# Performance work log

Hardware: AMD Instinct MI355X
Metric: run time of the kernel (lower is better)

## Reference

```python
import jax, jax.numpy as jnp
import numpy as np

N_HEAD = 16
LN_EPS = 1e-5


def setup_inputs() -> dict:
    key = jax.random.key(0)
    ks = jax.random.split(key, 12)
    B, S, D = 4, 1024, 1024
    s = 1.0 / np.sqrt(D)
    return {
        "Q": jax.random.normal(ks[0], (B, S, D), jnp.float32),
        "K": jax.random.normal(ks[1], (B, S, D), jnp.float32),
        "V": jax.random.normal(ks[2], (B, S, D), jnp.float32),
        # Linear weights stored torch-style [out, in]
        "Wq": jax.random.normal(ks[3], (D, D), jnp.float32) * s,
        "bq": jnp.zeros((D,), jnp.float32),
        "Wk": jax.random.normal(ks[4], (D, D), jnp.float32) * s,
        "bk": jnp.zeros((D,), jnp.float32),
        "Wv": jax.random.normal(ks[5], (D, D), jnp.float32) * s,
        "bv": jnp.zeros((D,), jnp.float32),
        "Wo": jax.random.normal(ks[6], (D, D), jnp.float32) * s,
        "bo": jnp.zeros((D,), jnp.float32),
        "ln_g": jnp.ones((D,), jnp.float32),
        "ln_b": jnp.zeros((D,), jnp.float32),
    }


def _layer_norm(x, g, b):
    mu = jnp.mean(x, axis=-1, keepdims=True)
    var = jnp.mean(jnp.square(x - mu), axis=-1, keepdims=True)
    return (x - mu) * jax.lax.rsqrt(var + LN_EPS) * g + b


def reference(Q, K, V, Wq, bq, Wk, bk, Wv, bv, Wo, bo, ln_g, ln_b):
    B, S, D = Q.shape
    H = N_HEAD
    dk = D // H
    # projections, split heads: [B, H, S, dk]
    q = (Q @ Wq.T + bq).reshape(B, S, H, dk).transpose(0, 2, 1, 3)
    k = (K @ Wk.T + bk).reshape(B, S, H, dk).transpose(0, 2, 1, 3)
    v = (V @ Wv.T + bv).reshape(B, S, H, dk).transpose(0, 2, 1, 3)
    scores = jnp.einsum("bhqd,bhkd->bhqk", q, k) / np.sqrt(dk)
    # NOTE: original module applies softmax twice (F.softmax then nn.Softmax)
    attn = jax.nn.softmax(jax.nn.softmax(scores, axis=-1), axis=-1)
    ctx = jnp.einsum("bhqk,bhkd->bhqd", attn, v)  # [B, H, S, dk]
    ctx = ctx.transpose(0, 2, 1, 3).reshape(B, S, D)
    out = ctx @ Wo.T + bo
    return _layer_norm(out + Q, ln_g, ln_b)
```

## Files before the change

### kernel.cpp

```cpp
#include <hip/hip_runtime.h>
#include <cstdint>
#include <cstddef>


typedef unsigned short ushort_t;
typedef __attribute__((ext_vector_type(8))) short bf16x8;
typedef __attribute__((ext_vector_type(8))) unsigned short us8;
typedef __attribute__((ext_vector_type(4))) unsigned short us4;
typedef __attribute__((ext_vector_type(4))) float f32x4;

#define MFMA16(a, b, c) __builtin_amdgcn_mfma_f32_16x16x32_bf16((a), (b), (c), 0, 0, 0)
#define EXP2F(x) __builtin_amdgcn_exp2f(x)
#define LOG2E 1.4426950408889634f

__device__ __forceinline__ float b2f(ushort_t u) {
  union { unsigned int i; float f; } x; x.i = ((unsigned int)u) << 16; return x.f;
}
__device__ __forceinline__ ushort_t f2b(float f) {
  union { unsigned int i; float f; } x; x.f = f;
  unsigned int r = (x.i + 0x7FFFu + ((x.i >> 16) & 1u)) >> 16;
  return (ushort_t)r;
}
__device__ __forceinline__ unsigned int cvtpk(float lo, float hi) {
  unsigned int r;
  asm("v_cvt_pk_bf16_f32 %0, %1, %2" : "=v"(r) : "v"(lo), "v"(hi));
  return r;
}
__device__ __forceinline__ us8 cvt8pk(float4 a, float4 b) {
  union { unsigned int u[4]; us8 v; } r;
  r.u[0] = cvtpk(a.x, a.y); r.u[1] = cvtpk(a.z, a.w);
  r.u[2] = cvtpk(b.x, b.y); r.u[3] = cvtpk(b.z, b.w);
  return r.v;
}

__device__ __forceinline__ void gll16(const ushort_t* g, ushort_t* l) {
  __builtin_amdgcn_global_load_lds(
      (const __attribute__((address_space(1))) void*)g,
      (__attribute__((address_space(3))) void*)l, 16, 0, 0);
}

__global__ __launch_bounds__(256, 8) void cvt4_kernel(
    const float* __restrict__ w0, const float* __restrict__ w1,
    const float* __restrict__ w2, const float* __restrict__ w3,
    ushort_t* __restrict__ dst) {
  const int which = blockIdx.y;
  const float* src = (which == 0) ? w0 : (which == 1) ? w1 : (which == 2) ? w2 : w3;
  const int i = (blockIdx.x * 256 + threadIdx.x) * 8;
  const float4 a = *(const float4*)(src + i);
  const float4 b = *(const float4*)(src + i + 4);
  *(us8*)(dst + (size_t)which * 1048576 + i) = cvt8pk(a, b);
}

__global__ __launch_bounds__(256, 3) void qkv_proj_kernel(
    const float* __restrict__ Qin, const float* __restrict__ Kin,
    const float* __restrict__ Vin,
    const ushort_t* __restrict__ wq, const ushort_t* __restrict__ wk,
    const ushort_t* __restrict__ wv,
    const float* __restrict__ bq, const float* __restrict__ bk,
    const float* __restrict__ bv,
    ushort_t* __restrict__ qb, ushort_t* __restrict__ kb,
    ushort_t* __restrict__ vb) {
  __shared__ __align__(16) ushort_t Asl0[128 * 32];
  __shared__ __align__(16) ushort_t Asl1[128 * 32];
  __shared__ __align__(16) ushort_t Bsl[3][128 * 32];
  const float* A; const ushort_t* W; const float* bias; float scale;
  if (blockIdx.z == 0)      { A = Qin; W = wq; bias = bq; scale = 0.125f * LOG2E; }
  else if (blockIdx.z == 1) { A = Kin; W = wk; bias = bk; scale = 1.0f; }
  else                      { A = Vin; W = wv; bias = bv; scale = 1.0f; }
  const int l = blockIdx.x;
  const int xcd = l & 7, ii = l >> 3;
  const int m0 = (xcd * 4 + (ii >> 3)) * 128;
  const int n0 = (ii & 7) * 128;
  const int tid = threadIdx.x;
  const int wave = tid >> 6, lane = tid & 63;
  const int l15 = lane & 15, quad = lane >> 4;
  const int wr = wave >> 1, wc = wave & 1;

  const int ra = tid >> 2, ca = (tid & 3) * 8;
  const float* Ap0 = A + (size_t)(m0 + ra) * 1024 + ca;
  const float* Ap1 = A + (size_t)(m0 + ra + 64) * 1024 + ca;

  const ushort_t* Bg0 = W + (size_t)(n0 + wave * 32 + (lane >> 2)) * 1024 + (lane & 3) * 8;
  const ushort_t* Bg1 = W + (size_t)(n0 + wave * 32 + 16 + (lane >> 2)) * 1024 + (lane & 3) * 8;
  ushort_t* Ba = Bsl[0];
  ushort_t* Bb = Bsl[1];
  ushort_t* Bc = Bsl[2];

  float4 xa0 = *(const float4*)(Ap0), xa1 = *(const float4*)(Ap0 + 4);
  float4 xa2 = *(const float4*)(Ap1), xa3 = *(const float4*)(Ap1 + 4);
  gll16(Bg0, Ba + wave * 1024);
  gll16(Bg1, Ba + wave * 1024 + 512);
  gll16(Bg0 + 32, Bb + wave * 1024);
  gll16(Bg1 + 32, Bb + wave * 1024 + 512);
  float4 ya0 = *(const float4*)(Ap0 + 32), ya1 = *(const float4*)(Ap0 + 36);
  float4 ya2 = *(const float4*)(Ap1 + 32), ya3 = *(const float4*)(Ap1 + 36);
  *(us8*)(Asl0 + ra * 32 + ca) = cvt8pk(xa0, xa1);
  *(us8*)(Asl0 + (ra + 64) * 32 + ca) = cvt8pk(xa2, xa3);
  asm volatile("s_waitcnt vmcnt(6) lgkmcnt(0)" ::: "memory");
  __builtin_amdgcn_s_barrier();

  f32x4 acc[4][4] = {};
#define QKV_COMPUTE(ASL, BSL)                                                   \
  {                                                                             \
    bf16x8 af[4], bfr[4];                                                       \
    _Pragma("unroll") for (int s = 0; s < 4; ++s)                               \
        af[s] = *(const bf16x8*)((ASL) + (wr * 64 + s * 16 + l15) * 32 + quad * 8); \
    _Pragma("unroll") for (int s = 0; s < 4; ++s)                               \
        bfr[s] = *(const bf16x8*)((BSL) + (wc * 64 + s * 16 + l15) * 32 + quad * 8); \
    _Pragma("unroll") for (int ms = 0; ms < 4; ++ms)                            \
        _Pragma("unroll") for (int ns = 0; ns < 4; ++ns)                        \
            acc[ms][ns] = MFMA16(af[ms], bfr[ns], acc[ms][ns]);                 \
  }

  for (int i = 0; i < 15; ++i) {
    const int k0 = i * 64;
    gll16(Bg0 + k0 + 64, Bc + wave * 1024);
    gll16(Bg1 + k0 + 64, Bc + wave * 1024 + 512);
    xa0 = *(const float4*)(Ap0 + k0 + 64); xa1 = *(const float4*)(Ap0 + k0 + 68);
    xa2 = *(const float4*)(Ap1 + k0 + 64); xa3 = *(const float4*)(Ap1 + k0 + 68);
    QKV_COMPUTE(Asl0, Ba)
    *(us8*)(Asl1 + ra * 32 + ca) = cvt8pk(ya0, ya1);
    *(us8*)(Asl1 + (ra + 64) * 32 + ca) = cvt8pk(ya2, ya3);
    asm volatile("s_waitcnt vmcnt(6) lgkmcnt(0)" ::: "memory");
    __builtin_amdgcn_s_barrier();
    gll16(Bg0 + k0 + 96, Ba + wave * 1024);
    gll16(Bg1 + k0 + 96, Ba + wave * 1024 + 512);
    ya0 = *(const float4*)(Ap0 + k0 + 96); ya1 = *(const float4*)(Ap0 + k0 + 100);
    ya2 = *(const float4*)(Ap1 + k0 + 96); ya3 = *(const float4*)(Ap1 + k0 + 100);
    QKV_COMPUTE(Asl1, Bb)
    *(us8*)(Asl0 + ra * 32 + ca) = cvt8pk(xa0, xa1);
    *(us8*)(Asl0 + (ra + 64) * 32 + ca) = cvt8pk(xa2, xa3);
    asm volatile("s_waitcnt vmcnt(6) lgkmcnt(0)" ::: "memory");
    __builtin_amdgcn_s_barrier();
    ushort_t* t = Ba; Ba = Bc; Bc = Bb; Bb = t;
  }
  QKV_COMPUTE(Asl0, Ba)
  *(us8*)(Asl1 + ra * 32 + ca) = cvt8pk(ya0, ya1);
  *(us8*)(Asl1 + (ra + 64) * 32 + ca) = cvt8pk(ya2, ya3);
  asm volatile("s_waitcnt vmcnt(0) lgkmcnt(0)" ::: "memory");
  __builtin_amdgcn_s_barrier();
  QKV_COMPUTE(Asl1, Bb)
#undef QKV_COMPUTE

  if (blockIdx.z != 2) {
    ushort_t* outp = (blockIdx.z == 0) ? qb : kb;
#pragma unroll
    for (int ns = 0; ns < 4; ++ns) {
      const int col = n0 + wc * 64 + ns * 16 + l15;
      const float bv_ = bias[col];
#pragma unroll
      for (int ms = 0; ms < 4; ++ms) {
        const int rowb = m0 + wr * 64 + ms * 16 + quad * 4;
#pragma unroll
        for (int r = 0; r < 4; ++r) {
          outp[(size_t)(rowb + r) * 1024 + col] =
              f2b((acc[ms][ns][r] + bv_) * scale);
        }
      }
    }
  } else {
#pragma unroll
    for (int ns = 0; ns < 4; ++ns) {
      const int col = n0 + wc * 64 + ns * 16 + l15;
      const float bv_ = bias[col];
      const int h = col >> 6, d = col & 63;
#pragma unroll
      for (int ms = 0; ms < 4; ++ms) {
        const int i0 = m0 + wr * 64 + ms * 16 + quad * 4;
        const int b = i0 >> 10, s0 = i0 & 1023;
        us4 pack;
#pragma unroll
        for (int r = 0; r < 4; ++r) pack[r] = f2b(acc[ms][ns][r] + bv_);
        *(us4*)(vb + ((size_t)(b * 16 + h) * 64 + d) * 1024 + s0) = pack;
      }
    }
  }
}

__global__ __launch_bounds__(256, 4) void attn_kernel(
    const ushort_t* __restrict__ qb, const ushort_t* __restrict__ kb,
    const ushort_t* __restrict__ vb, ushort_t* __restrict__ ctx) {
  __shared__ __align__(16) ushort_t Sh0[64 * 72];
  __shared__ __align__(16) ushort_t Sh1[64 * 72];
  __shared__ __align__(16) ushort_t Sh2[64 * 72];
  __shared__ __align__(16) ushort_t Sh3[64 * 72];

  const int tid = threadIdx.x, wave = tid >> 6, lane = tid & 63;
  const int l15 = lane & 15, quad = lane >> 4;
  const int l = blockIdx.x;
  const int xcd = l & 7, ii = l >> 3;
  const int bh = xcd * 8 + (ii >> 4);
  const int q0 = (ii & 15) * 64;
  const int b = bh >> 4, h = bh & 15;
  const ushort_t* qg = qb + ((size_t)b << 20) + h * 64;
  const ushort_t* kg = kb + ((size_t)b << 20) + h * 64;
  const ushort_t* vg = vb + ((size_t)bh << 16);

  const int kr0 = tid >> 3, kc0 = (tid & 7) * 8;
  const int kr1 = (tid + 256) >> 3, kc1 = kc0;
  const int o0 = kr0 * 72 + kc0, o1 = kr1 * 72 + kc1;

  *(us8*)(Sh0 + o0) = *(const us8*)(qg + (size_t)(q0 + kr0) * 1024 + kc0);
  *(us8*)(Sh0 + o1) = *(const us8*)(qg + (size_t)(q0 + kr1) * 1024 + kc1);
  us8 rk0 = *(const us8*)(kg + (size_t)kr0 * 1024 + kc0);
  us8 rk1 = *(const us8*)(kg + (size_t)kr1 * 1024 + kc1);
  *(us8*)(Sh1 + o0) = rk0;
  *(us8*)(Sh1 + o1) = rk1;
  rk0 = *(const us8*)(kg + (size_t)(64 + kr0) * 1024 + kc0);
  rk1 = *(const us8*)(kg + (size_t)(64 + kr1) * 1024 + kc1);
  __syncthreads();
  bf16x8 aqh[2];
  aqh[0] = *(const bf16x8*)(Sh0 + (wave * 16 + l15) * 72 + quad * 8);
  aqh[1] = *(const bf16x8*)(Sh0 + (wave * 16 + l15) * 72 + 32 + quad * 8);

  float z1 = 0.f;
  for (int kt = 0; kt < 16; ++kt) {
    const ushort_t* kcur = (kt & 1) ? Sh2 : Sh1;
    f32x4 sc[4] = {};
#pragma unroll
    for (int kk = 0; kk < 2; ++kk) {
#pragma unroll
      for (int ns = 0; ns < 4; ++ns) {
        const bf16x8 kf = *(const bf16x8*)(kcur + (ns * 16 + l15) * 72 + kk * 32 + quad * 8);
        sc[ns] = MFMA16(kf, aqh[kk], sc[ns]);
      }
    }
    if (kt < 15) {
      ushort_t* knxt = (kt & 1) ? Sh1 : Sh2;
      *(us8*)(knxt + o0) = rk0;
      *(us8*)(knxt + o1) = rk1;
      if (kt < 14) {
        rk0 = *(const us8*)(kg + (size_t)((kt + 2) * 64 + kr0) * 1024 + kc0);
        rk1 = *(const us8*)(kg + (size_t)((kt + 2) * 64 + kr1) * 1024 + kc1);
      }
    }
#pragma unroll
    for (int ns = 0; ns < 4; ++ns)
#pragma unroll
      for (int r = 0; r < 4; ++r) z1 += EXP2F(sc[ns][r]);
    asm volatile("s_waitcnt lgkmcnt(0)" ::: "memory");
    __builtin_amdgcn_s_barrier();
  }
  z1 += __shfl_xor(z1, 16, 64);
  z1 += __shfl_xor(z1, 32, 64);
  const float iz1 = LOG2E / z1;

  const int adr0 = ((((quad & 1) << 1) * 16) + l15) << 2;
  const int adr1 = adr0 + 64;

  f32x4 oac[4] = {};
  float z2 = 0.f;
  rk0 = *(const us8*)(kg + (size_t)kr0 * 1024 + kc0);
  rk1 = *(const us8*)(kg + (size_t)kr1 * 1024 + kc1);
  us8 rv0 = *(const us8*)(vg + (size_t)kr0 * 1024 + kc0);
  us8 rv1 = *(const us8*)(vg + (size_t)kr1 * 1024 + kc1);
  *(us8*)(Sh0 + o0) = rk0;
  *(us8*)(Sh0 + o1) = rk1;
  *(us8*)(Sh2 + o0) = rv0;
  *(us8*)(Sh2 + o1) = rv1;
  rk0 = *(const us8*)(kg + (size_t)(64 + kr0) * 1024 + kc0);
  rk1 = *(const us8*)(kg + (size_t)(64 + kr1) * 1024 + kc1);
  rv0 = *(const us8*)(vg + (size_t)kr0 * 1024 + 64 + kc0);
  rv1 = *(const us8*)(vg + (size_t)kr1 * 1024 + 64 + kc1);
  asm volatile("s_waitcnt lgkmcnt(0)" ::: "memory");
  __builtin_amdgcn_s_barrier();

  for (int kt = 0; kt < 16; ++kt) {
    const ushort_t* kcur = (kt & 1) ? Sh1 : Sh0;
    const ushort_t* vcur = (kt & 1) ? Sh3 : Sh2;
    f32x4 sc[4] = {};
#pragma unroll
    for (int kk = 0; kk < 2; ++kk) {
#pragma unroll
      for (int ns = 0; ns < 4; ++ns) {
        const bf16x8 kf = *(const bf16x8*)(kcur + (ns * 16 + l15) * 72 + kk * 32 + quad * 8);
        sc[ns] = MFMA16(kf, aqh[kk], sc[ns]);
      }
    }
    if (kt < 15) {
      ushort_t* knxt = (kt & 1) ? Sh0 : Sh1;
      ushort_t* vnxt = (kt & 1) ? Sh2 : Sh3;
      *(us8*)(knxt + o0) = rk0;
      *(us8*)(knxt + o1) = rk1;
      *(us8*)(vnxt + o0) = rv0;
      *(us8*)(vnxt + o1) = rv1;
      if (kt < 14) {
        rk0 = *(const us8*)(kg + (size_t)((kt + 2) * 64 + kr0) * 1024 + kc0);
        rk1 = *(const us8*)(kg + (size_t)((kt + 2) * 64 + kr1) * 1024 + kc1);
        rv0 = *(const us8*)(vg + (size_t)kr0 * 1024 + (kt + 2) * 64 + kc0);
        rv1 = *(const us8*)(vg + (size_t)kr1 * 1024 + (kt + 2) * 64 + kc1);
      }
    }
    unsigned int D[4][2];
#pragma unroll
    for (int ns = 0; ns < 4; ++ns) {
      const float e0 = EXP2F(EXP2F(sc[ns][0]) * iz1);
      const float e1 = EXP2F(EXP2F(sc[ns][1]) * iz1);
      const float e2 = EXP2F(EXP2F(sc[ns][2]) * iz1);
      const float e3 = EXP2F(EXP2F(sc[ns][3]) * iz1);
      z2 += (e0 + e1) + (e2 + e3);
      D[ns][0] = cvtpk(e0, e1);
      D[ns][1] = cvtpk(e2, e3);
    }
#pragma unroll
    for (int kk = 0; kk < 2; ++kk) {
      union { unsigned int u[4]; bf16x8 v; } pf;
#pragma unroll
      for (int t = 0; t < 4; ++t) {
        const int adr = (t >> 1) ? adr1 : adr0;
        const int lo = __builtin_amdgcn_ds_bpermute(adr, (int)D[2 * kk][t & 1]);
        const int hi = __builtin_amdgcn_ds_bpermute(adr, (int)D[2 * kk + 1][t & 1]);
        pf.u[t] = (unsigned int)((quad >= 2) ? hi : lo);
      }
#pragma unroll
      for (int ns2 = 0; ns2 < 4; ++ns2) {
        const bf16x8 vf = *(const bf16x8*)(vcur + (ns2 * 16 + l15) * 72 + kk * 32 + quad * 8);
        oac[ns2] = MFMA16(vf, pf.v, oac[ns2]);
      }
    }
    asm volatile("s_waitcnt lgkmcnt(0)" ::: "memory");
    __builtin_amdgcn_s_barrier();
  }

  z2 += __shfl_xor(z2, 16, 64);
  z2 += __shfl_xor(z2, 32, 64);
  const int s = q0 + wave * 16 + l15;
  ushort_t* crow = ctx + ((size_t)(b * 1024 + s)) * 1024 + h * 64;
#pragma unroll
  for (int ns2 = 0; ns2 < 4; ++ns2) {
    us4 pack;
#pragma unroll
    for (int r = 0; r < 4; ++r) pack[r] = f2b(oac[ns2][r] / z2);
    *(us4*)(crow + ns2 * 16 + quad * 4) = pack;
  }
}

__global__ __launch_bounds__(256, 4) void out_proj_kernel(
    const ushort_t* __restrict__ ctxp, const ushort_t* __restrict__ wo,
    const float* __restrict__ bo, ushort_t* __restrict__ pre) {
  __shared__ __align__(16) ushort_t Abuf[3][64 * 32];
  __shared__ __align__(16) ushort_t Bbuf[3][128 * 32];
  const int tid = threadIdx.x;
  const int wave = tid >> 6, lane = tid & 63;
  const int l15 = lane & 15, quad = lane >> 4;
  const int wr = wave >> 1, wc = wave & 1;
  const int l = blockIdx.x;
  const int xcd = l & 7, ii = l >> 3;
  const int m0 = (xcd * 8 + (ii >> 3)) * 64;
  const int n0 = (ii & 7) * 128;

  const ushort_t* Ag = ctxp + (size_t)(m0 + wave * 16 + (lane >> 2)) * 1024 + (lane & 3) * 8;
  const ushort_t* Bg0 = wo + (size_t)(n0 + wave * 32 + (lane >> 2)) * 1024 + (lane & 3) * 8;
  const ushort_t* Bg1 = wo + (size_t)(n0 + wave * 32 + 16 + (lane >> 2)) * 1024 + (lane & 3) * 8;

  ushort_t* Aa = Abuf[0]; ushort_t* Ab = Abuf[1]; ushort_t* Ac = Abuf[2];
  ushort_t* Ba = Bbuf[0]; ushort_t* Bb = Bbuf[1]; ushort_t* Bc = Bbuf[2];

  gll16(Ag, Aa + wave * 512);
  gll16(Bg0, Ba + wave * 1024);
  gll16(Bg1, Ba + wave * 1024 + 512);
  gll16(Ag + 32, Ab + wave * 512);
  gll16(Bg0 + 32, Bb + wave * 1024);
  gll16(Bg1 + 32, Bb + wave * 1024 + 512);
  asm volatile("s_waitcnt vmcnt(3)" ::: "memory");
  __builtin_amdgcn_s_barrier();

  f32x4 acc[2][4] = {};
#define OUTP_COMPUTE(ASL, BSL)                                                  \
  {                                                                             \
    bf16x8 af[2], bfr[4];                                                       \
    _Pragma("unroll") for (int s = 0; s < 2; ++s)                               \
        af[s] = *(const bf16x8*)((ASL) + (wr * 32 + s * 16 + l15) * 32 + quad * 8); \
    _Pragma("unroll") for (int s = 0; s < 4; ++s)                               \
        bfr[s] = *(const bf16x8*)((BSL) + (wc * 64 + s * 16 + l15) * 32 + quad * 8); \
    _Pragma("unroll") for (int ms = 0; ms < 2; ++ms)                            \
        _Pragma("unroll") for (int ns = 0; ns < 4; ++ns)                        \
            acc[ms][ns] = MFMA16(af[ms], bfr[ns], acc[ms][ns]);                 \
  }

  for (int p = 0; p < 30; ++p) {
    const int k = p * 32;
    gll16(Ag + k + 64, Ac + wave * 512);
    gll16(Bg0 + k + 64, Bc + wave * 1024);
    gll16(Bg1 + k + 64, Bc + wave * 1024 + 512);
    OUTP_COMPUTE(Aa, Ba)
    asm volatile("s_waitcnt vmcnt(3) lgkmcnt(0)" ::: "memory");
    __builtin_amdgcn_s_barrier();
    ushort_t* ta = Aa; Aa = Ab; Ab = Ac; Ac = ta;
    ushort_t* tb = Ba; Ba = Bb; Bb = Bc; Bc = tb;
  }
  OUTP_COMPUTE(Aa, Ba)
  asm volatile("s_waitcnt vmcnt(0) lgkmcnt(0)" ::: "memory");
  __builtin_amdgcn_s_barrier();
  OUTP_COMPUTE(Ab, Bb)
#undef OUTP_COMPUTE

#pragma unroll
  for (int ns = 0; ns < 4; ++ns) {
    const int col = n0 + wc * 64 + ns * 16 + l15;
    const float bv_ = bo[col];
#pragma unroll
    for (int ms = 0; ms < 2; ++ms) {
      const int rowb = m0 + wr * 32 + ms * 16 + quad * 4;
#pragma unroll
      for (int r = 0; r < 4; ++r) {
        pre[(size_t)(rowb + r) * 1024 + col] = f2b(acc[ms][ns][r] + bv_);
      }
    }
  }
}

__global__ __launch_bounds__(256, 4) void ln_kernel(
    const ushort_t* __restrict__ pre, const float* __restrict__ Q,
    const float* __restrict__ g, const float* __restrict__ bta,
    float* __restrict__ out) {
  const int row = blockIdx.x;
  const int tid = threadIdx.x;
  const size_t base = (size_t)row * 1024 + tid * 4;
  const ushort4 p4 = *(const ushort4*)(pre + base);
  const float4 q4 = *(const float4*)(Q + base);
  float v[4] = {b2f(p4.x) + q4.x, b2f(p4.y) + q4.y,
                b2f(p4.z) + q4.z, b2f(p4.w) + q4.w};
  float s1 = v[0] + v[1] + v[2] + v[3];
  float s2 = v[0]*v[0] + v[1]*v[1] + v[2]*v[2] + v[3]*v[3];
#pragma unroll
  for (int off = 1; off < 64; off <<= 1) {
    s1 += __shfl_xor(s1, off, 64);
    s2 += __shfl_xor(s2, off, 64);
  }
  __shared__ float r1[4], r2[4];
  const int wave = tid >> 6, lane = tid & 63;
  if (lane == 0) { r1[wave] = s1; r2[wave] = s2; }
  __syncthreads();
  const float t1 = r1[0] + r1[1] + r1[2] + r1[3];
  const float t2 = r2[0] + r2[1] + r2[2] + r2[3];
  const float mu = t1 * (1.0f / 1024.0f);
  const float var = t2 * (1.0f / 1024.0f) - mu * mu;
  const float inv = rsqrtf(var + 1e-5f);
  const int c0 = tid * 4;
#pragma unroll
  for (int j = 0; j < 4; ++j) {
    const int c = c0 + j;
    out[(size_t)row * 1024 + c] = (v[j] - mu) * inv * g[c] + bta[c];
  }
}

extern "C" void kernel_launch(void* const* d_in, const int* in_sizes, int n_in,
                              void* d_out, int out_size, void* d_ws, size_t ws_size,
                              hipStream_t stream) {
  const float* Q  = (const float*)d_in[0];
  const float* K  = (const float*)d_in[1];
  const float* V  = (const float*)d_in[2];
  const float* Wq = (const float*)d_in[3];
  const float* bq = (const float*)d_in[4];
  const float* Wk = (const float*)d_in[5];
  const float* bk = (const float*)d_in[6];
  const float* Wv = (const float*)d_in[7];
  const float* bv = (const float*)d_in[8];
  const float* Wo = (const float*)d_in[9];
  const float* bo = (const float*)d_in[10];
  const float* lg = (const float*)d_in[11];
  const float* lb = (const float*)d_in[12];

  char* ws = (char*)d_ws;
  ushort_t* qb  = (ushort_t*)(ws);
  ushort_t* kb  = (ushort_t*)(ws + ((size_t)8  << 20));
  ushort_t* vb  = (ushort_t*)(ws + ((size_t)16 << 20));
  ushort_t* pre = (ushort_t*)(ws);

  ushort_t* dptr  = (ushort_t*)d_out;
  ushort_t* wo_bf = dptr;
  ushort_t* wq_bf = dptr + 1048576;
  ushort_t* wk_bf = dptr + 2097152;
  ushort_t* wv_bf = dptr + 3145728;
  ushort_t* ctx   = dptr + 4194304;
  float*    out   = (float*)d_out;

  cvt4_kernel<<<dim3(512, 4), 256, 0, stream>>>(Wo, Wq, Wk, Wv, dptr);
  qkv_proj_kernel<<<dim3(256, 1, 3), 256, 0, stream>>>(Q, K, V, wq_bf, wk_bf, wv_bf,
                                                       bq, bk, bv, qb, kb, vb);
  attn_kernel<<<dim3(1024), 256, 0, stream>>>(qb, kb, vb, ctx);
  out_proj_kernel<<<dim3(512), 256, 0, stream>>>(ctx, wo_bf, bo, pre);
  ln_kernel<<<dim3(4096), 256, 0, stream>>>(pre, Q, lg, lb, out);
}
```

Before: 237.9 us.

## Load QKV weight fragments directly into registers instead of staging in LDS

The QKV projection kernel no longer stages weight tiles through a triple-buffered shared-memory ring filled by global-to-LDS loads. Each wave now reads its MFMA B fragments straight from global memory into registers, double-buffered across the two K halves. This cuts LDS use and LDS read traffic, which may allow higher occupancy. In exchange, weight data is loaded redundantly by the two waves sharing a column block, the loads are strided rather than coalesced, and more registers are needed.

```diff
diff --git a/kernel.cpp b/kernel.cpp
--- a/kernel.cpp
+++ b/kernel.cpp
@@ -62,7 +62,6 @@
     ushort_t* __restrict__ vb) {
   __shared__ __align__(16) ushort_t Asl0[128 * 32];
   __shared__ __align__(16) ushort_t Asl1[128 * 32];
-  __shared__ __align__(16) ushort_t Bsl[3][128 * 32];
   const float* A; const ushort_t* W; const float* bias; float scale;
   if (blockIdx.z == 0)      { A = Qin; W = wq; bias = bq; scale = 0.125f * LOG2E; }
   else if (blockIdx.z == 1) { A = Kin; W = wk; bias = bk; scale = 1.0f; }
@@ -80,66 +79,67 @@
   const float* Ap0 = A + (size_t)(m0 + ra) * 1024 + ca;
   const float* Ap1 = A + (size_t)(m0 + ra + 64) * 1024 + ca;
 
-  const ushort_t* Bg0 = W + (size_t)(n0 + wave * 32 + (lane >> 2)) * 1024 + (lane & 3) * 8;
-  const ushort_t* Bg1 = W + (size_t)(n0 + wave * 32 + 16 + (lane >> 2)) * 1024 + (lane & 3) * 8;
-  ushort_t* Ba = Bsl[0];
-  ushort_t* Bb = Bsl[1];
-  ushort_t* Bc = Bsl[2];
+  const ushort_t* Bp0 = W + (size_t)(n0 + wc * 64 +  0 + l15) * 1024 + quad * 8;
+  const ushort_t* Bp1 = W + (size_t)(n0 + wc * 64 + 16 + l15) * 1024 + quad * 8;
+  const ushort_t* Bp2 = W + (size_t)(n0 + wc * 64 + 32 + l15) * 1024 + quad * 8;
+  const ushort_t* Bp3 = W + (size_t)(n0 + wc * 64 + 48 + l15) * 1024 + quad * 8;
 
   float4 xa0 = *(const float4*)(Ap0), xa1 = *(const float4*)(Ap0 + 4);
   float4 xa2 = *(const float4*)(Ap1), xa3 = *(const float4*)(Ap1 + 4);
-  gll16(Bg0, Ba + wave * 1024);
-  gll16(Bg1, Ba + wave * 1024 + 512);
-  gll16(Bg0 + 32, Bb + wave * 1024);
-  gll16(Bg1 + 32, Bb + wave * 1024 + 512);
+  us8 bx0 = *(const us8*)(Bp0), bx1 = *(const us8*)(Bp1);
+  us8 bx2 = *(const us8*)(Bp2), bx3 = *(const us8*)(Bp3);
+  *(us8*)(Asl0 + ra * 32 + ca) = cvt8pk(xa0, xa1);
+  *(us8*)(Asl0 + (ra + 64) * 32 + ca) = cvt8pk(xa2, xa3);
   float4 ya0 = *(const float4*)(Ap0 + 32), ya1 = *(const float4*)(Ap0 + 36);
   float4 ya2 = *(const float4*)(Ap1 + 32), ya3 = *(const float4*)(Ap1 + 36);
-  *(us8*)(Asl0 + ra * 32 + ca) = cvt8pk(xa0, xa1);
-  *(us8*)(Asl0 + (ra + 64) * 32 + ca) = cvt8pk(xa2, xa3);
-  asm volatile("s_waitcnt vmcnt(6) lgkmcnt(0)" ::: "memory");
+  us8 by0 = *(const us8*)(Bp0 + 32), by1 = *(const us8*)(Bp1 + 32);
+  us8 by2 = *(const us8*)(Bp2 + 32), by3 = *(const us8*)(Bp3 + 32);
+  asm volatile("s_waitcnt lgkmcnt(0)" ::: "memory");
   __builtin_amdgcn_s_barrier();
 
   f32x4 acc[4][4] = {};
-#define QKV_COMPUTE(ASL, BSL)                                                   \
+#define QKV_COMPUTE(ASL, B0, B1, B2, B3)                                        \
   {                                                                             \
-    bf16x8 af[4], bfr[4];                                                       \
+    bf16x8 af[4];                                                               \
     _Pragma("unroll") for (int s = 0; s < 4; ++s)                               \
         af[s] = *(const bf16x8*)((ASL) + (wr * 64 + s * 16 + l15) * 32 + quad * 8); \
-    _Pragma("unroll") for (int s = 0; s < 4; ++s)                               \
-        bfr[s] = *(const bf16x8*)((BSL) + (wc * 64 + s * 16 + l15) * 32 + quad * 8); \
-    _Pragma("unroll") for (int ms = 0; ms < 4; ++ms)                            \
-        _Pragma("unroll") for (int ns = 0; ns < 4; ++ns)                        \
-            acc[ms][ns] = MFMA16(af[ms], bfr[ns], acc[ms][ns]);                 \
+    const bf16x8 bfr0 = (bf16x8)(B0), bfr1 = (bf16x8)(B1);                      \
+    const bf16x8 bfr2 = (bf16x8)(B2), bfr3 = (bf16x8)(B3);                      \
+    _Pragma("unroll") for (int ms = 0; ms < 4; ++ms) {                          \
+      acc[ms][0] = MFMA16(af[ms], bfr0, acc[ms][0]);                            \
+      acc[ms][1] = MFMA16(af[ms], bfr1, acc[ms][1]);                            \
+      acc[ms][2] = MFMA16(af[ms], bfr2, acc[ms][2]);                            \
+      acc[ms][3] = MFMA16(af[ms], bfr3, acc[ms][3]);                            \
+    }                                                                           \
   }
 
   for (int i = 0; i < 15; ++i) {
     const int k0 = i * 64;
-    gll16(Bg0 + k0 + 64, Bc + wave * 1024);
-    gll16(Bg1 + k0 + 64, Bc + wave * 1024 + 512);
     xa0 = *(const float4*)(Ap0 + k0 + 64); xa1 = *(const float4*)(Ap0 + k0 + 68);
     xa2 = *(const float4*)(Ap1 + k0 + 64); xa3 = *(const float4*)(Ap1 + k0 + 68);
-    QKV_COMPUTE(Asl0, Ba)
+    QKV_COMPUTE(Asl0, bx0, bx1, bx2, bx3)
+    bx0 = *(const us8*)(Bp0 + k0 + 64); bx1 = *(const us8*)(Bp1 + k0 + 64);
+    bx2 = *(const us8*)(Bp2 + k0 + 64); bx3 = *(const us8*)(Bp3 + k0 + 64);
     *(us8*)(Asl1 + ra * 32 + ca) = cvt8pk(ya0, ya1);
     *(us8*)(Asl1 + (ra + 64) * 32 + ca) = cvt8pk(ya2, ya3);
-    asm volatile("s_waitcnt vmcnt(6) lgkmcnt(0)" ::: "memory");
+    asm volatile("s_waitcnt lgkmcnt(0)" ::: "memory");
     __builtin_amdgcn_s_barrier();
-    gll16(Bg0 + k0 + 96, Ba + wave * 1024);
-    gll16(Bg1 + k0 + 96, Ba + wave * 1024 + 512);
     ya0 = *(const float4*)(Ap0 + k0 + 96); ya1 = *(const float4*)(Ap0 + k0 + 100);
     ya2 = *(const float4*)(Ap1 + k0 + 96); ya3 = *(const float4*)(Ap1 + k0 + 100);
-    QKV_COMPUTE(Asl1, Bb)
+    QKV_COMPUTE(Asl1, by0, by1, by2, by3)
+    by0 = *(const us8*)(Bp0 + k0 + 96); by1 = *(const us8*)(Bp1 + k0 + 96);
+    by2 = *(const us8*)(Bp2 + k0 + 96); by3 = *(const us8*)(Bp3 + k0 + 96);
     *(us8*)(Asl0 + ra * 32 + ca) = cvt8pk(xa0, xa1);
     *(us8*)(Asl0 + (ra + 64) * 32 + ca) = cvt8pk(xa2, xa3);
-    asm volatile("s_waitcnt vmcnt(6) lgkmcnt(0)" ::: "memory");
+    asm volatile("s_waitcnt lgkmcnt(0)" ::: "memory");
     __builtin_amdgcn_s_barrier();
-    ushort_t* t = Ba; Ba = Bc; Bc = Bb; Bb = t;
-  }
-  QKV_COMPUTE(Asl0, Ba)
+  }
+  QKV_COMPUTE(Asl0, bx0, bx1, bx2, bx3)
   *(us8*)(Asl1 + ra * 32 + ca) = cvt8pk(ya0, ya1);
   *(us8*)(Asl1 + (ra + 64) * 32 + ca) = cvt8pk(ya2, ya3);
-  asm volatile("s_waitcnt vmcnt(0) lgkmcnt(0)" ::: "memory");
+  asm volatile("s_waitcnt lgkmcnt(0)" ::: "memory");
   __builtin_amdgcn_s_barrier();
-  QKV_COMPUTE(Asl1, Bb)
+  QKV_COMPUTE(Asl1, by0, by1, by2, by3)
 #undef QKV_COMPUTE
 
   if (blockIdx.z != 2) {
```

Result: slower. 255.6 us (+7.4%).
